# Performance work log

Measured on AMD Instinct MI355X. Metric: run time of the kernel, lower is better.

Reference implementation:

```python
import jax, jax.numpy as jnp
import numpy as np

H = 64   # hidden_size
K = 20   # number of attention groups


def _gru_layer(x, Wih, Whh, bih, bhh):
    # x: [B, T, I] -> [B, T, H]; PyTorch GRU gate order (r, z, n)
    xw = x @ Wih.T + bih  # [B, T, 3H]
    h0 = jnp.zeros((x.shape[0], Whh.shape[1]), x.dtype)

    def step(h, xt):
        gh = h @ Whh.T + bhh
        xr, xz, xn = jnp.split(xt, 3, axis=-1)
        hr, hz, hn = jnp.split(gh, 3, axis=-1)
        r = jax.nn.sigmoid(xr + hr)
        z = jax.nn.sigmoid(xz + hz)
        n = jnp.tanh(xn + r * hn)
        h = (1.0 - z) * n + z * h
        return h, h

    _, hs = jax.lax.scan(step, h0, jnp.swapaxes(xw, 0, 1))
    return jnp.swapaxes(hs, 0, 1)


def setup_inputs():
    key = jax.random.key(0)
    ks = iter(jax.random.split(key, 40))

    def p(shape, fan_in):
        s = 1.0 / np.sqrt(fan_in)
        return jax.random.uniform(next(ks), shape, jnp.float32, -s, s)

    N, T, D = 10240, 60, 6  # N = K * m with m = 512
    inp = {"x": jax.random.normal(next(ks), (N, T, D), jnp.float32)}
    inp.update(
        rnn_Wih0=p((3 * H, D), D), rnn_Whh0=p((3 * H, H), H),
        rnn_bih0=p((3 * H,), H), rnn_bhh0=p((3 * H,), H),
        rnn_Wih1=p((3 * H, H), H), rnn_Whh1=p((3 * H, H), H),
        rnn_bih1=p((3 * H,), H), rnn_bhh1=p((3 * H,), H),
        trans_W=p((H, H), H), trans_b=p((H,), H),
        a=jax.random.normal(next(ks), (2 * H, 1), jnp.float32),
        fc_W=p((H, H), H), fc_b=p((H,), H),
        fco_W=p((1, H), H), fco_b=p((1,), H),
        al_in_W=p((H, H), H), al_in_b=p((H,), H),
        al_Wih0=p((3 * H, H), H), al_Whh0=p((3 * H, H), H),
        al_bih0=p((3 * H,), H), al_bhh0=p((3 * H,), H),
        al_Wih1=p((3 * H, H), H), al_Whh1=p((3 * H, H), H),
        al_bih1=p((3 * H,), H), al_bhh1=p((3 * H,), H),
        al_att1_W=p((H // 2, H), H), al_att1_b=p((H // 2,), H),
        al_att2_W=p((1, H // 2), H // 2),
        al_out_W=p((1, 2 * H), 2 * H), al_out_b=p((1,), 2 * H),
    )
    return inp


def reference(x, rnn_Wih0, rnn_Whh0, rnn_bih0, rnn_bhh0,
              rnn_Wih1, rnn_Whh1, rnn_bih1, rnn_bhh1,
              trans_W, trans_b, a, fc_W, fc_b, fco_W, fco_b,
              al_in_W, al_in_b,
              al_Wih0, al_Whh0, al_bih0, al_bhh0,
              al_Wih1, al_Whh1, al_bih1, al_bhh1,
              al_att1_W, al_att1_b, al_att2_W, al_out_W, al_out_b):
    # ---- 2-layer GRU encoder over time ----
    out = _gru_layer(x, rnn_Wih0, rnn_Whh0, rnn_bih0, rnn_bhh0)
    out = _gru_layer(out, rnn_Wih1, rnn_Whh1, rnn_bih1, rnn_bhh1)
    h = out[:, -1, :].reshape(K, -1, H)  # [K, m, H]

    # ---- dense all-pairs GAT attention (split-projection form of a^T [x_j ; x_i]) ----
    xp = h @ trans_W.T + trans_b         # transformation(x) == transformation(y)
    s_dst = xp @ a[:H, 0]                # contributes along column index j
    s_src = xp @ a[H:, 0]                # contributes along row index i
    score = jax.nn.leaky_relu(s_src[:, :, None] + s_dst[:, None, :])  # [K, m, m]
    att = jax.nn.softmax(score, axis=2)
    h = jnp.einsum('kij,kjd->kid', att, h) + h
    h = h @ fc_W.T + fc_b
    h = jnp.swapaxes(h, 0, 1)            # [m, K, H]  (K acts as seq len for ALSTM)

    # ---- ALSTM (inference: dropout inactive) ----
    z = jnp.tanh(h @ al_in_W.T + al_in_b)
    r = _gru_layer(z, al_Wih0, al_Whh0, al_bih0, al_bhh0)
    r = _gru_layer(r, al_Wih1, al_Whh1, al_bih1, al_bhh1)
    att_s = jax.nn.softmax(jnp.tanh(r @ al_att1_W.T + al_att1_b) @ al_att2_W.T, axis=1)  # [m, K, 1]
    out_att = jnp.sum(r * att_s, axis=1)
    alstm_out = (jnp.concatenate([r[:, -1, :], out_att], axis=1) @ al_out_W.T + al_out_b)[:, 0]

    pred = (jax.nn.leaky_relu(h[:, -1, :]) @ fco_W.T + fco_b)[:, 0]
    return (alstm_out, pred)
```

## Files before the change

kernel.cpp:

```cpp
#include <hip/hip_runtime.h>

#define DEV __device__ __forceinline__

DEV float fast_rcp(float x) {
#if __has_builtin(__builtin_amdgcn_rcpf)
  return __builtin_amdgcn_rcpf(x);
#else
  return 1.0f / x;
#endif
}
DEV float sigm(float x) { return fast_rcp(1.0f + __expf(-x)); }
DEV float tanh_f(float x) {
  float e = __expf(-2.0f * fabsf(x));
  float t = 1.0f - 2.0f * e * fast_rcp(1.0f + e);
  return copysignf(t, x);
}
DEV float lrelu(float x) { return x > 0.0f ? x : 0.01f * x; }

DEV float wave_sum(float v) {
#pragma unroll
  for (int m = 32; m; m >>= 1) v += __shfl_xor(v, m);
  return v;
}
DEV float wave_max(float v) {
#pragma unroll
  for (int m = 32; m; m >>= 1) v = fmaxf(v, __shfl_xor(v, m));
  return v;
}
DEV float dot4(float4 w, float4 x, float acc) {
  acc = fmaf(w.x, x.x, acc);
  acc = fmaf(w.y, x.y, acc);
  acc = fmaf(w.z, x.z, acc);
  acc = fmaf(w.w, x.w, acc);
  return acc;
}

DEV float bcast(float v, int lane) {
  return __int_as_float(__builtin_amdgcn_readlane(__float_as_int(v), lane));
}

constexpr int E_SPW = 5;
constexpr int E_WAVES = 8;
constexpr int L_W0 = 0;
constexpr int L_W1 = 12288;
constexpr int E_DW = 36864;
constexpr int E_LDS = E_DW * 4;

__launch_bounds__(512)
__global__ void gru2_enc(const float* __restrict__ x,
                         const float* __restrict__ w3e0,
                         const float* __restrict__ w3e1,
                         const float* __restrict__ bih0, const float* __restrict__ bhh0,
                         const float* __restrict__ bih1, const float* __restrict__ bhh1,
                         float* __restrict__ h_out) {
  extern __shared__ float lds[];
  const int tid = threadIdx.x;
  const int wave = tid >> 6;
  const int j = tid & 63;
  const int j3 = j * 3;

  {
    const float4* s0 = (const float4*)(w3e0 + 6 * 192);
    for (int i = tid; i < 12288 / 4; i += 512) ((float4*)(lds + L_W0))[i] = s0[i];
    const float4* s1 = (const float4*)w3e1;
    for (int i = tid; i < 24576 / 4; i += 512) ((float4*)(lds + L_W1))[i] = s1[i];
  }
  float wx0[6][3];
#pragma unroll
  for (int k = 0; k < 6; ++k)
#pragma unroll
    for (int g = 0; g < 3; ++g) wx0[k][g] = w3e0[k * 192 + j3 + g];

  const float br0 = bih0[j] + bhh0[j];
  const float bz0 = bih0[64 + j] + bhh0[64 + j];
  const float bxn0 = bih0[128 + j];
  const float bhn0 = bhh0[128 + j];
  const float br1 = bih1[j] + bhh1[j];
  const float bz1 = bih1[64 + j] + bhh1[64 + j];
  const float bxn1 = bih1[128 + j];
  const float bhn1 = bhh1[128 + j];

  float h0r[E_SPW], h1r[E_SPW];
#pragma unroll
  for (int s = 0; s < E_SPW; ++s) { h0r[s] = 0.0f; h1r[s] = 0.0f; }
  __syncthreads();

  const int seq0 = blockIdx.x * (E_WAVES * E_SPW) + wave * E_SPW;
  const int si = j / 6;
  const int ci = j - si * 6;
  const bool xlane = (j < 6 * E_SPW);
  const float* xg = x + (size_t)(seq0 + si) * 360 + ci;

  float xcur = xlane ? xg[0] : 0.0f;

  for (int t = 0; t < 60; ++t) {
    float xnext = (xlane && t + 1 < 60) ? xg[(size_t)(t + 1) * 6] : 0.0f;

    float ar[E_SPW], az[E_SPW], anx[E_SPW], anh[E_SPW];
#pragma unroll
    for (int s = 0; s < E_SPW; ++s) { ar[s] = 0.f; az[s] = 0.f; anx[s] = 0.f; anh[s] = 0.f; }

#pragma clang loop unroll_count(4)
    for (int k = 0; k < 64; ++k) {
      const int wb = L_W0 + k * 192 + j3;
      const float wr = lds[wb], wz = lds[wb + 1], wn = lds[wb + 2];
#pragma unroll
      for (int s = 0; s < E_SPW; ++s) {
        const float hk = bcast(h0r[s], k);
        ar[s] = fmaf(wr, hk, ar[s]);
        az[s] = fmaf(wz, hk, az[s]);
        anh[s] = fmaf(wn, hk, anh[s]);
      }
    }
#pragma unroll
    for (int s = 0; s < E_SPW; ++s) {
#pragma unroll
      for (int c = 0; c < 6; ++c) {
        const float xk = bcast(xcur, s * 6 + c);
        ar[s] = fmaf(wx0[c][0], xk, ar[s]);
        az[s] = fmaf(wx0[c][1], xk, az[s]);
        anx[s] = fmaf(wx0[c][2], xk, anx[s]);
      }
    }
#pragma unroll
    for (int s = 0; s < E_SPW; ++s) {
      float r = sigm(ar[s] + br0);
      float z = sigm(az[s] + bz0);
      float n = tanh_f(anx[s] + bxn0 + r * (anh[s] + bhn0));
      h0r[s] = (1.0f - z) * n + z * h0r[s];
    }

#pragma unroll
    for (int s = 0; s < E_SPW; ++s) { ar[s] = 0.f; az[s] = 0.f; anx[s] = 0.f; anh[s] = 0.f; }
#pragma clang loop unroll_count(4)
    for (int k = 0; k < 64; ++k) {
      const int wb = L_W1 + k * 192 + j3;
      const float wr = lds[wb], wz = lds[wb + 1], wn = lds[wb + 2];
#pragma unroll
      for (int s = 0; s < E_SPW; ++s) {
        const float hk = bcast(h0r[s], k);
        ar[s] = fmaf(wr, hk, ar[s]);
        az[s] = fmaf(wz, hk, az[s]);
        anx[s] = fmaf(wn, hk, anx[s]);
      }
    }
#pragma clang loop unroll_count(4)
    for (int k = 0; k < 64; ++k) {
      const int wb = L_W1 + (64 + k) * 192 + j3;
      const float wr = lds[wb], wz = lds[wb + 1], wn = lds[wb + 2];
#pragma unroll
      for (int s = 0; s < E_SPW; ++s) {
        const float hk = bcast(h1r[s], k);
        ar[s] = fmaf(wr, hk, ar[s]);
        az[s] = fmaf(wz, hk, az[s]);
        anh[s] = fmaf(wn, hk, anh[s]);
      }
    }
#pragma unroll
    for (int s = 0; s < E_SPW; ++s) {
      float r = sigm(ar[s] + br1);
      float z = sigm(az[s] + bz1);
      float n = tanh_f(anx[s] + bxn1 + r * (anh[s] + bhn1));
      h1r[s] = (1.0f - z) * n + z * h1r[s];
    }
    xcur = xnext;
  }

#pragma unroll
  for (int s = 0; s < E_SPW; ++s)
    h_out[(size_t)(seq0 + s) * 64 + j] = h1r[s];
}

constexpr int A_W_DW = 128 * 192;
constexpr int A_WAVES = 8;
constexpr int A_LDS = (A_W_DW + A_WAVES * 128) * 4;

__launch_bounds__(512, 2)
__global__ void gru1(const float* __restrict__ xin,
                     const float* __restrict__ w3,
                     const float* __restrict__ bih, const float* __restrict__ bhh,
                     int T,
                     float* __restrict__ rout) {
  extern __shared__ float lds[];
  const int tid = threadIdx.x;
  const int wave = tid >> 6;
  const int j = tid & 63;
  const int j3 = j * 3;
  const int XB = A_W_DW + wave * 128;

  {
    const float4* sp = (const float4*)w3;
    for (int i = tid; i < A_W_DW / 4; i += 512) ((float4*)lds)[i] = sp[i];
  }
  const float br = bih[j] + bhh[j];
  const float bz = bih[64 + j] + bhh[64 + j];
  const float bxn = bih[128 + j];
  const float bhn = bhh[128 + j];

  float hr = 0.0f;
  lds[XB + 64 + j] = 0.0f;
  __syncthreads();

  const int seq = blockIdx.x * A_WAVES + wave;
  const float* xs = xin + (size_t)seq * T * 64;

#define A_QUAD(WROW0, HOFF, AN)                                            \
  {                                                                        \
    float4 hv = *(const float4*)&lds[XB + (HOFF)];                         \
    _Pragma("unroll") for (int c = 0; c < 4; ++c) {                        \
      const float wr = lds[((WROW0) + c) * 192 + j3];                      \
      const float wz = lds[((WROW0) + c) * 192 + j3 + 1];                  \
      const float wn = lds[((WROW0) + c) * 192 + j3 + 2];                  \
      const float hc = (c == 0) ? hv.x : (c == 1) ? hv.y                   \
                      : (c == 2) ? hv.z : hv.w;                            \
      ar = fmaf(wr, hc, ar);                                               \
      az = fmaf(wz, hc, az);                                               \
      AN = fmaf(wn, hc, AN);                                               \
    }                                                                      \
  }

  float xcur = xs[j];
  for (int t = 0; t < T; ++t) {
    float xnext = (t + 1 < T) ? xs[(size_t)(t + 1) * 64 + j] : 0.0f;
    lds[XB + j] = xcur;

    float ar = 0.f, az = 0.f, anx = 0.f, anh = 0.f;
#pragma unroll
    for (int kq = 0; kq < 16; ++kq) A_QUAD(kq * 4, kq * 4, anx);
#pragma unroll
    for (int kq = 0; kq < 16; ++kq) A_QUAD(64 + kq * 4, 64 + kq * 4, anh);

    float r = sigm(ar + br);
    float z = sigm(az + bz);
    float n = tanh_f(anx + bxn + r * (anh + bhn));
    float h = (1.0f - z) * n + z * hr;
    hr = h;
    lds[XB + 64 + j] = h;
    rout[((size_t)seq * T + t) * 64 + j] = h;
    xcur = xnext;
  }
#undef A_QUAD
}

__global__ void w3_prep(const float* __restrict__ Wih0, const float* __restrict__ Whh0,
                        const float* __restrict__ Wih1, const float* __restrict__ Whh1,
                        const float* __restrict__ aWih0, const float* __restrict__ aWhh0,
                        const float* __restrict__ aWih1, const float* __restrict__ aWhh1,
                        float* __restrict__ d_e0, float* __restrict__ d_e1,
                        float* __restrict__ d_a0, float* __restrict__ d_a1) {
  const int sec = blockIdx.x >> 3;
  const int bi = blockIdx.x & 7;
  const float* Wih; const float* Whh; float* dst; int I;
  if (sec == 0)      { Wih = Wih0;  Whh = Whh0;  dst = d_e0; I = 6; }
  else if (sec == 1) { Wih = Wih1;  Whh = Whh1;  dst = d_e1; I = 64; }
  else if (sec == 2) { Wih = aWih0; Whh = aWhh0; dst = d_a0; I = 64; }
  else               { Wih = aWih1; Whh = aWhh1; dst = d_a1; I = 64; }
  const int tot = (I + 64) * 192;
  for (int idx = bi * blockDim.x + threadIdx.x; idx < tot; idx += 8 * blockDim.x) {
    const int k = idx / 192;
    const int rem = idx - k * 192;
    const int jj = rem / 3;
    const int g = rem - jj * 3;
    dst[idx] = (k < I) ? Wih[(g * 64 + jj) * I + k] : Whh[(g * 64 + jj) * 64 + (k - I)];
  }
}

__global__ void gat_prep(const float* __restrict__ tW, const float* __restrict__ tb,
                         const float* __restrict__ a, float* __restrict__ vbuf) {
  const int d = threadIdx.x;
  float vd = 0.0f, vs = 0.0f;
  for (int e = 0; e < 64; ++e) {
    float w = tW[e * 64 + d];
    vd = fmaf(w, a[e], vd);
    vs = fmaf(w, a[64 + e], vs);
  }
  vbuf[d] = vd;
  vbuf[64 + d] = vs;
  if (d == 0) {
    float cd = 0.0f, cs = 0.0f;
    for (int e = 0; e < 64; ++e) {
      cd = fmaf(tb[e], a[e], cd);
      cs = fmaf(tb[e], a[64 + e], cs);
    }
    vbuf[128] = cd;
    vbuf[129] = cs;
  }
}

__global__ void gat_svals(const float* __restrict__ h_enc, const float* __restrict__ vbuf,
                          float* __restrict__ s_src, float* __restrict__ s_dst) {
  const int wave = (blockIdx.x * blockDim.x + threadIdx.x) >> 6;
  const int lane = threadIdx.x & 63;
  float h = h_enc[(size_t)wave * 64 + lane];
  float pd = h * vbuf[lane];
  float ps = h * vbuf[64 + lane];
  pd = wave_sum(pd);
  ps = wave_sum(ps);
  if (lane == 0) {
    s_dst[wave] = pd + vbuf[128];
    s_src[wave] = ps + vbuf[129];
  }
}

__launch_bounds__(256)
__global__ void gat_attn(const float* __restrict__ h_enc,
                         const float* __restrict__ s_src,
                         const float* __restrict__ s_dst,
                         float* __restrict__ hout) {
  const int k = blockIdx.x >> 7;
  const int tile = blockIdx.x & 127;
  const int wv = threadIdx.x >> 6;
  const int lane = threadIdx.x & 63;
  const int i = tile * 4 + wv;
  __shared__ float sdbuf[512];
  __shared__ __align__(16) float pbuf[4][512];

  for (int u = threadIdx.x; u < 512; u += 256) sdbuf[u] = s_dst[k * 512 + u];
  __syncthreads();

  const float si = s_src[k * 512 + i];
  float ev[8];
  float mx = -1e30f;
#pragma unroll
  for (int u = 0; u < 8; ++u) {
    ev[u] = lrelu(si + sdbuf[lane + u * 64]);
    mx = fmaxf(mx, ev[u]);
  }
  mx = wave_max(mx);
  float lsum = 0.0f;
#pragma unroll
  for (int u = 0; u < 8; ++u) {
    float p = __expf(ev[u] - mx);
    pbuf[wv][lane + u * 64] = p;
    lsum += p;
  }
  lsum = wave_sum(lsum);
  const float inv = fast_rcp(lsum);

  const float* hk = h_enc + (size_t)k * 512 * 64;
  const float4* pv = (const float4*)pbuf[wv];
  float acc0 = 0.0f, acc1 = 0.0f;
#pragma unroll 2
  for (int jj = 0; jj < 128; ++jj) {
    float4 p = pv[jj];
    const float* hp = hk + (size_t)(jj * 4) * 64 + lane;
    acc0 = fmaf(p.x, hp[0], acc0);
    acc1 = fmaf(p.y, hp[64], acc1);
    acc0 = fmaf(p.z, hp[128], acc0);
    acc1 = fmaf(p.w, hp[192], acc1);
  }
  hout[((size_t)k * 512 + i) * 64 + lane] =
      (acc0 + acc1) * inv + hk[(size_t)i * 64 + lane];
}

__launch_bounds__(256)
__global__ void gat_out(const float* __restrict__ hin,
                        const float* __restrict__ fcW, const float* __restrict__ fcb,
                        const float* __restrict__ fcoW, const float* __restrict__ fcob,
                        const float* __restrict__ alinW, const float* __restrict__ alinb,
                        float* __restrict__ zout, float* __restrict__ pred) {
  const int wv = threadIdx.x >> 6;
  const int lane = threadIdx.x & 63;
  const int n = blockIdx.x * 4 + wv;
  const int k = n >> 9;
  const int i = n & 511;
  __shared__ __align__(16) float rbuf[4][64];
  __shared__ __align__(16) float rbuf2[4][64];

  float4 fw[16], aw[16];
  {
    const float4* p1 = (const float4*)(fcW + lane * 64);
    const float4* p2 = (const float4*)(alinW + lane * 64);
#pragma unroll
    for (int kk = 0; kk < 16; ++kk) fw[kk] = p1[kk];
#pragma unroll
    for (int kk = 0; kk < 16; ++kk) aw[kk] = p2[kk];
  }

  rbuf[wv][lane] = hin[(size_t)n * 64 + lane];
  float h2 = fcb[lane];
  const float4* rv = (const float4*)rbuf[wv];
#pragma unroll
  for (int kk = 0; kk < 16; ++kk) h2 = dot4(fw[kk], rv[kk], h2);

  if (k == 19) {
    float pv = lrelu(h2) * fcoW[lane];
    pv = wave_sum(pv);
    if (lane == 0) pred[i] = pv + fcob[0];
  }

  rbuf2[wv][lane] = h2;
  float zz = alinb[lane];
  const float4* rv2 = (const float4*)rbuf2[wv];
#pragma unroll
  for (int kk = 0; kk < 16; ++kk) zz = dot4(aw[kk], rv2[kk], zz);
  zout[((size_t)i * 20 + k) * 64 + lane] = tanh_f(zz);
}

__launch_bounds__(256)
__global__ void alstm_head(const float* __restrict__ r1,
                           const float* __restrict__ W1,
                           const float* __restrict__ b1,
                           const float* __restrict__ W2,
                           const float* __restrict__ Wo,
                           const float* __restrict__ bo,
                           float* __restrict__ alstm_out) {
  const int wv = threadIdx.x >> 6;
  const int lane = threadIdx.x & 63;
  const int i = blockIdx.x * 4 + wv;
  const int e = lane & 31;
  __shared__ __align__(16) float rbuf[4][64];
  __shared__ float scb[4][20];

  float4 w1r[16];
  {
    const float4* p = (const float4*)(W1 + e * 64);
#pragma unroll
    for (int kk = 0; kk < 16; ++kk) w1r[kk] = p[kk];
  }
  const float b1e = b1[e];
  const float w2e = W2[e];

  for (int k = 0; k < 20; ++k) {
    rbuf[wv][lane] = r1[((size_t)i * 20 + k) * 64 + lane];
    float u = b1e;
    const float4* rp = (const float4*)rbuf[wv];
#pragma unroll
    for (int kk = 0; kk < 16; ++kk) u = dot4(w1r[kk], rp[kk], u);
    u = tanh_f(u) * w2e;
#pragma unroll
    for (int m = 16; m; m >>= 1) u += __shfl_xor(u, m);
    if (lane == 0) scb[wv][k] = u;
  }

  float mx = -1e30f;
#pragma unroll
  for (int k = 0; k < 20; ++k) mx = fmaxf(mx, scb[wv][k]);
  float p[20];
  float l = 0.0f;
#pragma unroll
  for (int k = 0; k < 20; ++k) {
    p[k] = __expf(scb[wv][k] - mx);
    l += p[k];
  }
  const float inv = fast_rcp(l);

  float oa = 0.0f, rlast = 0.0f;
#pragma unroll
  for (int k = 0; k < 20; ++k) {
    float rv = r1[((size_t)i * 20 + k) * 64 + lane];
    oa = fmaf(p[k], rv, oa);
    if (k == 19) rlast = rv;
  }
  oa *= inv;
  float v = fmaf(Wo[lane], rlast, Wo[64 + lane] * oa);
  v = wave_sum(v);
  if (lane == 0) alstm_out[i] = v + bo[0];
}

extern "C" void kernel_launch(void* const* d_in, const int* in_sizes, int n_in,
                              void* d_out, int out_size, void* d_ws, size_t ws_size,
                              hipStream_t stream) {
  const float* x      = (const float*)d_in[0];
  const float* Wih0   = (const float*)d_in[1];
  const float* Whh0   = (const float*)d_in[2];
  const float* bih0   = (const float*)d_in[3];
  const float* bhh0   = (const float*)d_in[4];
  const float* Wih1   = (const float*)d_in[5];
  const float* Whh1   = (const float*)d_in[6];
  const float* bih1   = (const float*)d_in[7];
  const float* bhh1   = (const float*)d_in[8];
  const float* transW = (const float*)d_in[9];
  const float* transb = (const float*)d_in[10];
  const float* a_vec  = (const float*)d_in[11];
  const float* fcW    = (const float*)d_in[12];
  const float* fcb    = (const float*)d_in[13];
  const float* fcoW   = (const float*)d_in[14];
  const float* fcob   = (const float*)d_in[15];
  const float* alinW  = (const float*)d_in[16];
  const float* alinb  = (const float*)d_in[17];
  const float* aWih0  = (const float*)d_in[18];
  const float* aWhh0  = (const float*)d_in[19];
  const float* abih0  = (const float*)d_in[20];
  const float* abhh0  = (const float*)d_in[21];
  const float* aWih1  = (const float*)d_in[22];
  const float* aWhh1  = (const float*)d_in[23];
  const float* abih1  = (const float*)d_in[24];
  const float* abhh1  = (const float*)d_in[25];
  const float* att1W  = (const float*)d_in[26];
  const float* att1b  = (const float*)d_in[27];
  const float* att2W  = (const float*)d_in[28];
  const float* aloutW = (const float*)d_in[29];
  const float* aloutb = (const float*)d_in[30];

  float* out = (float*)d_out;

  float* W = (float*)d_ws;
  float* h_enc = W; W += 10240 * 64;
  float* vbuf  = W; W += 256;
  float* s_src = W; W += 10240;
  float* s_dst = W; W += 10240;
  float* hout  = W; W += 10240 * 64;
  float* zbuf  = W; W += 512 * 20 * 64;
  float* r1    = W; W += 512 * 20 * 64;
  float* w3a0  = W; W += 24576;
  float* w3a1  = W; W += 24576;
  float* w3e0 = zbuf;
  float* w3e1 = zbuf + 13440;

  static bool attr_done = false;
  if (!attr_done) {
    hipFuncSetAttribute((const void*)gru2_enc,
                        hipFuncAttributeMaxDynamicSharedMemorySize, E_LDS);
    hipFuncSetAttribute((const void*)gru1,
                        hipFuncAttributeMaxDynamicSharedMemorySize, A_LDS);
    attr_done = true;
  }

  w3_prep<<<32, 256, 0, stream>>>(Wih0, Whh0, Wih1, Whh1, aWih0, aWhh0,
                                  aWih1, aWhh1, w3e0, w3e1, w3a0, w3a1);
  gru2_enc<<<256, 512, E_LDS, stream>>>(x, w3e0, w3e1, bih0, bhh0, bih1,
                                        bhh1, h_enc);
  gat_prep<<<1, 64, 0, stream>>>(transW, transb, a_vec, vbuf);
  gat_svals<<<2560, 256, 0, stream>>>(h_enc, vbuf, s_src, s_dst);
  gat_attn<<<2560, 256, 0, stream>>>(h_enc, s_src, s_dst, hout);
  gat_out<<<2560, 256, 0, stream>>>(hout, fcW, fcb, fcoW, fcob, alinW, alinb,
                                    zbuf, out + 512);
  gru1<<<64, 512, A_LDS, stream>>>(zbuf, w3a0, abih0, abhh0, 20, h_enc);
  gru1<<<64, 512, A_LDS, stream>>>(h_enc, w3a1, abih1, abhh1, 20, r1);
  alstm_head<<<128, 256, 0, stream>>>(r1, att1W, att1b, att2W, aloutW, aloutb,
                                      out);
}
```

Measured before the change: 1.416 ms.

## Stage encoder hidden states in LDS and read them as float4 instead of readlane broadcasts

The encoder GRU matvec used to broadcast each hidden element with readlane, which is a scalar-path operation, once per k and per sequence. It now writes each wave's hidden states to LDS in [k][s] interleaved order and reads them back as float4 vectors, with weights repacked so r/z load as a float2 plus a separate n load. The last 12 rows of the layer-0 hidden weights are held in registers to save LDS. This trades readlane traffic for LDS reads and adds more LDS and register pressure.

```diff
diff --git a/kernel.cpp b/kernel.cpp
--- a/kernel.cpp
+++ b/kernel.cpp
@@ -1,6 +1,8 @@
 #include <hip/hip_runtime.h>
 
 #define DEV __device__ __forceinline__
+
+typedef float f2 __attribute__((ext_vector_type(2)));
 
 DEV float fast_rcp(float x) {
 #if __has_builtin(__builtin_amdgcn_rcpf)
@@ -42,14 +44,62 @@
 constexpr int E_SPW = 5;
 constexpr int E_WAVES = 8;
 constexpr int L_W0 = 0;
-constexpr int L_W1 = 12288;
-constexpr int E_DW = 36864;
+constexpr int L_W1 = 9984;
+constexpr int L_HB = 34560;
+constexpr int E_DW = 40704;
 constexpr int E_LDS = E_DW * 4;
+
+#define PAIR_FMA(WRa, WZa, WNa, WRb, WZb, WNb, HB, M, AN)                    \
+  {                                                                          \
+    const float4 hq0 = *(const float4*)&lds[(HB) + (M) * 12];                \
+    const float4 hq1 = *(const float4*)&lds[(HB) + (M) * 12 + 4];            \
+    const float4 hq2 = *(const float4*)&lds[(HB) + (M) * 12 + 8];            \
+    ar[0] = fmaf(WRa, hq0.x, ar[0]); az[0] = fmaf(WZa, hq0.x, az[0]);        \
+    AN[0] = fmaf(WNa, hq0.x, AN[0]);                                         \
+    ar[1] = fmaf(WRa, hq0.y, ar[1]); az[1] = fmaf(WZa, hq0.y, az[1]);        \
+    AN[1] = fmaf(WNa, hq0.y, AN[1]);                                         \
+    ar[2] = fmaf(WRa, hq0.z, ar[2]); az[2] = fmaf(WZa, hq0.z, az[2]);        \
+    AN[2] = fmaf(WNa, hq0.z, AN[2]);                                         \
+    ar[3] = fmaf(WRa, hq0.w, ar[3]); az[3] = fmaf(WZa, hq0.w, az[3]);        \
+    AN[3] = fmaf(WNa, hq0.w, AN[3]);                                         \
+    ar[4] = fmaf(WRa, hq1.x, ar[4]); az[4] = fmaf(WZa, hq1.x, az[4]);        \
+    AN[4] = fmaf(WNa, hq1.x, AN[4]);                                         \
+    ar[0] = fmaf(WRb, hq1.z, ar[0]); az[0] = fmaf(WZb, hq1.z, az[0]);        \
+    AN[0] = fmaf(WNb, hq1.z, AN[0]);                                         \
+    ar[1] = fmaf(WRb, hq1.w, ar[1]); az[1] = fmaf(WZb, hq1.w, az[1]);        \
+    AN[1] = fmaf(WNb, hq1.w, AN[1]);                                         \
+    ar[2] = fmaf(WRb, hq2.x, ar[2]); az[2] = fmaf(WZb, hq2.x, az[2]);        \
+    AN[2] = fmaf(WNb, hq2.x, AN[2]);                                         \
+    ar[3] = fmaf(WRb, hq2.y, ar[3]); az[3] = fmaf(WZb, hq2.y, az[3]);        \
+    AN[3] = fmaf(WNb, hq2.y, AN[3]);                                         \
+    ar[4] = fmaf(WRb, hq2.z, ar[4]); az[4] = fmaf(WZb, hq2.z, az[4]);        \
+    AN[4] = fmaf(WNb, hq2.z, AN[4]);                                         \
+  }
+
+#define PAIR_LDS(WBASE, M, HB, AN)                                           \
+  {                                                                          \
+    const int ra_ = (WBASE) + (2 * (M)) * 192;                               \
+    const int rb_ = ra_ + 192;                                               \
+    const f2 wa_ = *(const f2*)&lds[ra_ + j2];                               \
+    const float wna_ = lds[ra_ + 128 + j];                                   \
+    const f2 wb_ = *(const f2*)&lds[rb_ + j2];                               \
+    const float wnb_ = lds[rb_ + 128 + j];                                   \
+    PAIR_FMA(wa_.x, wa_.y, wna_, wb_.x, wb_.y, wnb_, HB, M, AN)              \
+  }
+
+#define XPART(S, ARx, AZx, ANXx)                       \
+  _Pragma("unroll") for (int c = 0; c < 6; ++c) {      \
+    const float xk = bcast(xcur, (S) * 6 + c);         \
+    ARx = fmaf(wx0[c][0], xk, ARx);                    \
+    AZx = fmaf(wx0[c][1], xk, AZx);                    \
+    ANXx = fmaf(wx0[c][2], xk, ANXx);                  \
+  }
 
 __launch_bounds__(512)
 __global__ void gru2_enc(const float* __restrict__ x,
                          const float* __restrict__ w3e0,
-                         const float* __restrict__ w3e1,
+                         const float* __restrict__ e2h0,
+                         const float* __restrict__ e2w1,
                          const float* __restrict__ bih0, const float* __restrict__ bhh0,
                          const float* __restrict__ bih1, const float* __restrict__ bhh1,
                          float* __restrict__ h_out) {
@@ -58,18 +108,25 @@
   const int wave = tid >> 6;
   const int j = tid & 63;
   const int j3 = j * 3;
+  const int j2 = j * 2;
+  const int h0base = L_HB + wave * 768;
+  const int h1base = h0base + 384;
 
   {
-    const float4* s0 = (const float4*)(w3e0 + 6 * 192);
-    for (int i = tid; i < 12288 / 4; i += 512) ((float4*)(lds + L_W0))[i] = s0[i];
-    const float4* s1 = (const float4*)w3e1;
+    const float4* s0 = (const float4*)e2h0;
+    for (int i = tid; i < 9984 / 4; i += 512) ((float4*)(lds + L_W0))[i] = s0[i];
+    const float4* s1 = (const float4*)e2w1;
     for (int i = tid; i < 24576 / 4; i += 512) ((float4*)(lds + L_W1))[i] = s1[i];
   }
-  float wx0[6][3];
+  float wx0[6][3], wh_hi[12][3];
 #pragma unroll
   for (int k = 0; k < 6; ++k)
 #pragma unroll
     for (int g = 0; g < 3; ++g) wx0[k][g] = w3e0[k * 192 + j3 + g];
+#pragma unroll
+  for (int r = 0; r < 12; ++r)
+#pragma unroll
+    for (int g = 0; g < 3; ++g) wh_hi[r][g] = w3e0[(58 + r) * 192 + j3 + g];
 
   const float br0 = bih0[j] + bhh0[j];
   const float bz0 = bih0[64 + j] + bhh0[64 + j];
@@ -83,6 +140,11 @@
   float h0r[E_SPW], h1r[E_SPW];
 #pragma unroll
   for (int s = 0; s < E_SPW; ++s) { h0r[s] = 0.0f; h1r[s] = 0.0f; }
+#pragma unroll
+  for (int s = 0; s < 6; ++s) {
+    lds[h0base + j * 6 + s] = 0.0f;
+    lds[h1base + j * 6 + s] = 0.0f;
+  }
   __syncthreads();
 
   const int seq0 = blockIdx.x * (E_WAVES * E_SPW) + wave * E_SPW;
@@ -100,28 +162,20 @@
 #pragma unroll
     for (int s = 0; s < E_SPW; ++s) { ar[s] = 0.f; az[s] = 0.f; anx[s] = 0.f; anh[s] = 0.f; }
 
-#pragma clang loop unroll_count(4)
-    for (int k = 0; k < 64; ++k) {
-      const int wb = L_W0 + k * 192 + j3;
-      const float wr = lds[wb], wz = lds[wb + 1], wn = lds[wb + 2];
-#pragma unroll
-      for (int s = 0; s < E_SPW; ++s) {
-        const float hk = bcast(h0r[s], k);
-        ar[s] = fmaf(wr, hk, ar[s]);
-        az[s] = fmaf(wz, hk, az[s]);
-        anh[s] = fmaf(wn, hk, anh[s]);
-      }
-    }
-#pragma unroll
-    for (int s = 0; s < E_SPW; ++s) {
-#pragma unroll
-      for (int c = 0; c < 6; ++c) {
-        const float xk = bcast(xcur, s * 6 + c);
-        ar[s] = fmaf(wx0[c][0], xk, ar[s]);
-        az[s] = fmaf(wx0[c][1], xk, az[s]);
-        anx[s] = fmaf(wx0[c][2], xk, anx[s]);
-      }
-    }
+#pragma clang loop unroll_count(2)
+    for (int m = 0; m < 26; ++m) PAIR_LDS(L_W0, m, h0base, anh)
+#pragma unroll
+    for (int p = 0; p < 6; ++p)
+      PAIR_FMA(wh_hi[2 * p][0], wh_hi[2 * p][1], wh_hi[2 * p][2],
+               wh_hi[2 * p + 1][0], wh_hi[2 * p + 1][1], wh_hi[2 * p + 1][2],
+               h0base, 26 + p, anh)
+
+    XPART(0, ar[0], az[0], anx[0])
+    XPART(1, ar[1], az[1], anx[1])
+    XPART(2, ar[2], az[2], anx[2])
+    XPART(3, ar[3], az[3], anx[3])
+    XPART(4, ar[4], az[4], anx[4])
+
 #pragma unroll
     for (int s = 0; s < E_SPW; ++s) {
       float r = sigm(ar[s] + br0);
@@ -129,33 +183,19 @@
       float n = tanh_f(anx[s] + bxn0 + r * (anh[s] + bhn0));
       h0r[s] = (1.0f - z) * n + z * h0r[s];
     }
+    {
+      *(f2*)&lds[h0base + j * 6] = (f2){h0r[0], h0r[1]};
+      *(f2*)&lds[h0base + j * 6 + 2] = (f2){h0r[2], h0r[3]};
+      lds[h0base + j * 6 + 4] = h0r[4];
+    }
 
 #pragma unroll
     for (int s = 0; s < E_SPW; ++s) { ar[s] = 0.f; az[s] = 0.f; anx[s] = 0.f; anh[s] = 0.f; }
-#pragma clang loop unroll_count(4)
-    for (int k = 0; k < 64; ++k) {
-      const int wb = L_W1 + k * 192 + j3;
-      const float wr = lds[wb], wz = lds[wb + 1], wn = lds[wb + 2];
-#pragma unroll
-      for (int s = 0; s < E_SPW; ++s) {
-        const float hk = bcast(h0r[s], k);
-        ar[s] = fmaf(wr, hk, ar[s]);
-        az[s] = fmaf(wz, hk, az[s]);
-        anx[s] = fmaf(wn, hk, anx[s]);
-      }
-    }
-#pragma clang loop unroll_count(4)
-    for (int k = 0; k < 64; ++k) {
-      const int wb = L_W1 + (64 + k) * 192 + j3;
-      const float wr = lds[wb], wz = lds[wb + 1], wn = lds[wb + 2];
-#pragma unroll
-      for (int s = 0; s < E_SPW; ++s) {
-        const float hk = bcast(h1r[s], k);
-        ar[s] = fmaf(wr, hk, ar[s]);
-        az[s] = fmaf(wz, hk, az[s]);
-        anh[s] = fmaf(wn, hk, anh[s]);
-      }
-    }
+#pragma clang loop unroll_count(2)
+    for (int m = 0; m < 32; ++m) PAIR_LDS(L_W1, m, h0base, anx)
+#pragma clang loop unroll_count(2)
+    for (int m = 0; m < 32; ++m) PAIR_LDS(L_W1 + 64 * 192, m, h1base, anh)
+
 #pragma unroll
     for (int s = 0; s < E_SPW; ++s) {
       float r = sigm(ar[s] + br1);
@@ -163,6 +203,12 @@
       float n = tanh_f(anx[s] + bxn1 + r * (anh[s] + bhn1));
       h1r[s] = (1.0f - z) * n + z * h1r[s];
     }
+    {
+      *(f2*)&lds[h1base + j * 6] = (f2){h1r[0], h1r[1]};
+      *(f2*)&lds[h1base + j * 6 + 2] = (f2){h1r[2], h1r[3]};
+      lds[h1base + j * 6 + 4] = h1r[4];
+    }
+
     xcur = xnext;
   }
 
@@ -246,22 +292,51 @@
                         const float* __restrict__ Wih1, const float* __restrict__ Whh1,
                         const float* __restrict__ aWih0, const float* __restrict__ aWhh0,
                         const float* __restrict__ aWih1, const float* __restrict__ aWhh1,
-                        float* __restrict__ d_e0, float* __restrict__ d_e1,
+                        float* __restrict__ d_e0, float* __restrict__ d_h0,
+                        float* __restrict__ d_w1,
                         float* __restrict__ d_a0, float* __restrict__ d_a1) {
   const int sec = blockIdx.x >> 3;
   const int bi = blockIdx.x & 7;
-  const float* Wih; const float* Whh; float* dst; int I;
-  if (sec == 0)      { Wih = Wih0;  Whh = Whh0;  dst = d_e0; I = 6; }
-  else if (sec == 1) { Wih = Wih1;  Whh = Whh1;  dst = d_e1; I = 64; }
-  else if (sec == 2) { Wih = aWih0; Whh = aWhh0; dst = d_a0; I = 64; }
-  else               { Wih = aWih1; Whh = aWhh1; dst = d_a1; I = 64; }
-  const int tot = (I + 64) * 192;
-  for (int idx = bi * blockDim.x + threadIdx.x; idx < tot; idx += 8 * blockDim.x) {
-    const int k = idx / 192;
-    const int rem = idx - k * 192;
-    const int jj = rem / 3;
-    const int g = rem - jj * 3;
-    dst[idx] = (k < I) ? Wih[(g * 64 + jj) * I + k] : Whh[(g * 64 + jj) * 64 + (k - I)];
+
+  if (sec == 0) {
+    for (int idx = bi * blockDim.x + threadIdx.x; idx < 70 * 192; idx += 8 * blockDim.x) {
+      const int k = idx / 192;
+      const int rem = idx - k * 192;
+      const int jj = rem / 3;
+      const int g = rem - jj * 3;
+      d_e0[idx] = (k < 6) ? Wih0[(g * 64 + jj) * 6 + k]
+                          : Whh0[(g * 64 + jj) * 64 + (k - 6)];
+    }
+  } else if (sec == 1) {
+    for (int idx = bi * blockDim.x + threadIdx.x; idx < 52 * 192; idx += 8 * blockDim.x) {
+      const int k = idx / 192;
+      const int rem = idx - k * 192;
+      int jj, g;
+      if (rem < 128) { jj = rem >> 1; g = rem & 1; }
+      else           { jj = rem - 128; g = 2; }
+      d_h0[idx] = Whh0[(g * 64 + jj) * 64 + k];
+    }
+  } else if (sec == 2) {
+    for (int idx = bi * blockDim.x + threadIdx.x; idx < 128 * 192; idx += 8 * blockDim.x) {
+      const int k = idx / 192;
+      const int rem = idx - k * 192;
+      int jj, g;
+      if (rem < 128) { jj = rem >> 1; g = rem & 1; }
+      else           { jj = rem - 128; g = 2; }
+      d_w1[idx] = (k < 64) ? Wih1[(g * 64 + jj) * 64 + k]
+                           : Whh1[(g * 64 + jj) * 64 + (k - 64)];
+    }
+  } else {
+    const float* Wih = (sec == 3) ? aWih0 : aWih1;
+    const float* Whh = (sec == 3) ? aWhh0 : aWhh1;
+    float* dst = (sec == 3) ? d_a0 : d_a1;
+    for (int idx = bi * blockDim.x + threadIdx.x; idx < 128 * 192; idx += 8 * blockDim.x) {
+      const int k = idx / 192;
+      const int rem = idx - k * 192;
+      const int jj = rem / 3;
+      const int g = rem - jj * 3;
+      dst[idx] = (k < 64) ? Wih[(g * 64 + jj) * 64 + k] : Whh[(g * 64 + jj) * 64 + (k - 64)];
+    }
   }
 }
 
@@ -506,7 +581,8 @@
   float* w3a0  = W; W += 24576;
   float* w3a1  = W; W += 24576;
   float* w3e0 = zbuf;
-  float* w3e1 = zbuf + 13440;
+  float* e2h0 = zbuf + 13440;
+  float* e2w1 = zbuf + 23424;
 
   static bool attr_done = false;
   if (!attr_done) {
@@ -517,10 +593,11 @@
     attr_done = true;
   }
 
-  w3_prep<<<32, 256, 0, stream>>>(Wih0, Whh0, Wih1, Whh1, aWih0, aWhh0,
-                                  aWih1, aWhh1, w3e0, w3e1, w3a0, w3a1);
-  gru2_enc<<<256, 512, E_LDS, stream>>>(x, w3e0, w3e1, bih0, bhh0, bih1,
-                                        bhh1, h_enc);
+  w3_prep<<<40, 256, 0, stream>>>(Wih0, Whh0, Wih1, Whh1, aWih0, aWhh0,
+                                  aWih1, aWhh1, w3e0, e2h0, e2w1,
+                                  w3a0, w3a1);
+  gru2_enc<<<256, 512, E_LDS, stream>>>(x, w3e0, e2h0, e2w1,
+                                        bih0, bhh0, bih1, bhh1, h_enc);
   gat_prep<<<1, 64, 0, stream>>>(transW, transb, a_vec, vbuf);
   gat_svals<<<2560, 256, 0, stream>>>(h_enc, vbuf, s_src, s_dst);
   gat_attn<<<2560, 256, 0, stream>>>(h_enc, s_src, s_dst, hout);
```

Measured after the change: 1.366 ms. -3.5%, faster.
